# Optimization experiments

Measured on AMD Instinct MI355X. Metric: run time of the kernel, lower is better.

The kernel has to match this reference:

```python
import jax, jax.numpy as jnp
import numpy as np
from jax import lax


def binarize(x):
    # sign() binarization with straight-through estimator (identity backward),
    # matching the BNN .data in-place trick in BinarizeConv2d / bilinear.
    return x + lax.stop_gradient(jnp.sign(x) - x)


def maxpool2x2(x):
    # NCHW 2x2 max pool, stride 2
    return lax.reduce_window(x, -jnp.inf, lax.max,
                             (1, 1, 2, 2), (1, 1, 2, 2), 'VALID')


def conv2d(x, w):
    # NCHW / OIHW valid conv, stride 1
    return lax.conv_general_dilated(x, w, (1, 1), 'VALID',
                                    dimension_numbers=('NCHW', 'OIHW', 'NCHW'))


def setup_inputs() -> dict:
    key = jax.random.key(0)
    ks = jax.random.split(key, 6)
    B = 16384
    x = jax.random.normal(ks[0], (B, 1, 32, 32), dtype=jnp.float32)
    w1 = jax.random.normal(ks[1], (6, 1, 5, 5), dtype=jnp.float32) * 0.2
    w2 = jax.random.normal(ks[2], (16, 6, 5, 5), dtype=jnp.float32) * 0.08
    wfc1 = jax.random.normal(ks[3], (120, 400), dtype=jnp.float32) * 0.05
    wfc2 = jax.random.normal(ks[4], (84, 120), dtype=jnp.float32) * 0.09
    wfc3 = jax.random.normal(ks[5], (10, 84), dtype=jnp.float32) * 0.1
    return {'x': x, 'w1': w1, 'w2': w2, 'wfc1': wfc1, 'wfc2': wfc2, 'wfc3': wfc3}


def reference(x, w1, w2, wfc1, wfc2, wfc3):
    # conv1 (binarized input + weights) -> pool
    h = maxpool2x2(conv2d(binarize(x), binarize(w1)))          # [B,6,14,14]
    # conv2 -> pool
    h = maxpool2x2(conv2d(binarize(h), binarize(w2)))          # [B,16,5,5]
    h = h.reshape(h.shape[0], -1)                              # [B,400]
    h = binarize(h) @ binarize(wfc1).T                         # [B,120]
    h = binarize(h) @ binarize(wfc2).T                         # [B,84]
    h = binarize(h) @ binarize(wfc3).T                         # [B,10]
    return h
```

## Files before the change

### kernel.cpp

```cpp
#include <hip/hip_runtime.h>
#include <hip/hip_bf16.h>

typedef unsigned int u32;
typedef unsigned short u16;
typedef unsigned long long u64;

#define OC1 0
#define OC2 8
#define WCONV 104
#define OF1 104
#define OF2 2024
#define OF3 2664
#define WTOT 2704

__global__ void pack_w(const float* __restrict__ w1, const float* __restrict__ w2,
                       const float* __restrict__ f1, const float* __restrict__ f2,
                       const float* __restrict__ f3, u64* __restrict__ P) {
    int g = blockIdx.x * 256 + threadIdx.x;
    if (g < 1920) {
        int j = g / 15, w = g % 15;
        u64 v = 0;
        if (w < 14 && j < 120) {
            bool sp = (w >= 7); int k = sp ? w - 7 : w;
            for (int f = 0; f < 4; f++) {
                int p = 4 * k + f;
                if (p < 25)
                    for (int ch = 0; ch < 16; ch++) {
                        float x = f1[j * 400 + ch * 25 + p];
                        bool b = sp ? (x < 0.0f) : (x != 0.0f);
                        if (b) v |= 1ull << (f * 16 + ch);
                    }
            }
        }
        P[OF1 + g] = v;
    } else if (g < 2560) {
        int g2 = g - 1920, j = g2 / 5, w = g2 % 5;
        u64 v = 0;
        if (w < 4 && j < 84) {
            bool sp = (w >= 2); int h = w & 1;
            for (int b = 0; b < 64; b++) {
                int k = h * 64 + b;
                if (k < 120) {
                    float x = f2[j * 120 + k];
                    bool bb = sp ? (x < 0.0f) : (x != 0.0f);
                    if (bb) v |= 1ull << b;
                }
            }
        }
        P[OF2 + g2] = v;
    } else if (g < 2600) {
        int g3 = g - 2560, j = g3 / 4, w = g3 % 4;
        bool sp = (w >= 2); int h = w & 1;
        u64 v = 0;
        for (int b = 0; b < 64; b++) {
            int k = h * 64 + b;
            if (k < 84) {
                float x = f3[j * 84 + k];
                bool bb = sp ? (x < 0.0f) : (x != 0.0f);
                if (bb) v |= 1ull << b;
            }
        }
        P[OF3 + g3] = v;
    } else if (g < 2696) {
        int c = g - 2600, ch = c / 6, w = c % 6;
        bool sp = (w >= 3); int wp = w % 3;
        u64 v = 0;
        for (int half = 0; half < 2; half++) {
            int r = 2 * wp + half;
            if (r < 5) {
                u32 rowv = 0;
                for (int ci = 0; ci < 6; ci++)
                    for (int cc = 0; cc < 5; cc++) {
                        float x = w2[((ch * 6 + ci) * 5 + r) * 5 + cc];
                        bool b = sp ? (x < 0.0f) : (x != 0.0f);
                        int bit = (ci < 3) ? (5 * ci + cc) : (15 + 5 * (ci - 3) + cc);
                        if (b) rowv |= 1u << bit;
                    }
                v |= (u64)rowv << (32 * half);
            }
        }
        P[OC2 + ch * 6 + (sp ? 3 : 0) + wp] = v;
    } else if (g < 2702) {
        int c = g - 2696;
        int pair = c % 3; bool sp = (c >= 3);
        u64 v = 0;
        for (int half = 0; half < 2; half++) {
            int ch = 2 * pair + half;
            u32 wd = 0;
            for (int r = 0; r < 5; r++)
                for (int cc = 0; cc < 5; cc++) {
                    float x = w1[ch * 25 + r * 5 + cc];
                    bool b = sp ? (x < 0.0f) : (x != 0.0f);
                    if (b) wd |= 1u << (6 * r + cc);
                }
            v |= (u64)wd << (32 * half);
        }
        P[OC1 + (sp ? 3 : 0) + pair] = v;
    }
}

#define G 8

__device__ __forceinline__ u32 sgnb(int v) { return (u32)v >> 31; }
__device__ __forceinline__ u32 nzb(int v)  { return (u32)(v | -v) >> 31; }
#define WB() __builtin_amdgcn_wave_barrier()

__global__ __launch_bounds__(256, 8) void lenet_main(const float* __restrict__ X,
                                                     const u64* __restrict__ P,
                                                     float* __restrict__ out) {
    __shared__ u32 xs[G][32], xn[G][32];
    __shared__ u64 h1An[G][14], h1As[G][14], h1Bn[G][14], h1Bs[G][14];
    __shared__ u64 h2n[G][7], h2s[G][7];
    __shared__ u64 f1s[G][2], f1n[G][2], f2s[G][2], f2n[G][2];

    const int tid = threadIdx.x;
    const int wid = tid >> 6, lane = tid & 63;
    const int img0 = blockIdx.x * G;
    const int liA = wid * 2, liB = liA + 1;
    const int li0 = liA;

    const float4* X4 = (const float4*)(X + (size_t)img0 * 1024);

    float4 rvA[4];
    #pragma unroll
    for (int it = 0; it < 4; it++) rvA[it] = X4[liA * 256 + it * 64 + lane];

    u64 db;
    {
        bool bad = false;
        if (lane < 51) {
            u64 w, exp;
            if (lane < 48) {
                int ch = lane / 3, k = lane % 3;
                w = P[OC2 + ch * 6 + k];
                exp = (k < 2) ? 0x3FFFFFFF3FFFFFFFull : 0x000000003FFFFFFFull;
            } else {
                w = P[OC1 + (lane - 48)];
                exp = 0x1F7DF7DF1F7DF7DFull;
            }
            bad = (w != exp);
        }
        db = __ballot(bad);
    }

    auto conv1_fast = [&](int li) {
        const int px = lane & 15;
        const int pxe = px < 14 ? px : 13;
        const int tt = 2 * pxe;
        const int g = lane >> 4;
        u64 c1s0 = P[OC1 + 3], c1s1 = P[OC1 + 4], c1s2 = P[OC1 + 5];
        #pragma unroll
        for (int it = 0; it < 4; it++) {
            int seg = it * 4 + g;
            int py = seg < 14 ? seg : 13;
            int oy = 2 * py;
            u32 rs[6];
            #pragma unroll
            for (int k = 0; k < 6; k++) rs[k] = xs[li][oy + k];
            u32 W6a = 0;
            #pragma unroll
            for (int r = 0; r < 5; r++) W6a |= ((rs[r] >> tt) & 63u) << (6 * r);
            u32 W6b = (W6a >> 6) | (((rs[5] >> tt) & 63u) << 24);
            u32 cnt[6];
            #pragma unroll
            for (int c = 0; c < 6; c++) cnt[c] = 255;
            #pragma unroll
            for (int dy = 0; dy < 2; dy++) {
                u32 base = dy ? W6b : W6a;
                #pragma unroll
                for (int dx = 0; dx < 2; dx++) {
                    u32 w = (dx ? (base >> 1) : base) & 0x1F7DF7DFu;
                    u64 W = ((u64)w << 32) | w;
                    u64 t0 = W ^ c1s0;
                    cnt[0] = min(cnt[0], (u32)__popc((u32)t0));
                    cnt[1] = min(cnt[1], (u32)__popc((u32)(t0 >> 32)));
                    u64 t1 = W ^ c1s1;
                    cnt[2] = min(cnt[2], (u32)__popc((u32)t1));
                    cnt[3] = min(cnt[3], (u32)__popc((u32)(t1 >> 32)));
                    u64 t2w = W ^ c1s2;
                    cnt[4] = min(cnt[4], (u32)__popc((u32)t2w));
                    cnt[5] = min(cnt[5], (u32)__popc((u32)(t2w >> 32)));
                }
            }
            u64 bS[6];
            #pragma unroll
            for (int c = 0; c < 6; c++) bS[c] = __ballot(cnt[c] >= 13);
            if (px == 0 && seg < 14) {
                int sh = lane & 48;
                u64 rAs = ((bS[0] >> sh) & 0x3FFF) | (((bS[1] >> sh) & 0x3FFF) << 16) | (((bS[2] >> sh) & 0x3FFF) << 32);
                u64 rBs = ((bS[3] >> sh) & 0x3FFF) | (((bS[4] >> sh) & 0x3FFF) << 16) | (((bS[5] >> sh) & 0x3FFF) << 32);
                h1As[li][seg] = rAs; h1Bs[li][seg] = rBs;
            }
        }
    };
    auto conv1_slow = [&](int li) {
        const int px = lane & 15;
        const int pxe = px < 14 ? px : 13;
        const int tt = 2 * pxe;
        const int g = lane >> 4;
        for (int it = 0; it < 4; it++) {
            int seg = it * 4 + g;
            int py = seg < 14 ? seg : 13;
            int oy = 2 * py;
            int best[6];
            for (int c = 0; c < 6; c++) best[c] = -1000;
            for (int dy = 0; dy < 2; dy++)
                for (int dx = 0; dx < 2; dx++) {
                    u32 wn = 0, ws = 0;
                    for (int r = 0; r < 5; r++) {
                        u32 an = xn[li][oy + dy + r], as = xs[li][oy + dy + r];
                        wn |= ((an >> (tt + dx)) & 31u) << (6 * r);
                        ws |= ((as >> (tt + dx)) & 31u) << (6 * r);
                    }
                    u64 Wn = ((u64)wn << 32) | wn;
                    u64 Ws = ((u64)ws << 32) | ws;
                    for (int p = 0; p < 3; p++) {
                        u64 cn = P[OC1 + p], cs = P[OC1 + 3 + p];
                        u64 m  = Wn & cn;
                        u64 mx = m & (Ws ^ cs);
                        int a0 = __popc((u32)m) - 2 * __popc((u32)mx);
                        int a1 = __popc((u32)(m >> 32)) - 2 * __popc((u32)(mx >> 32));
                        best[2 * p]     = max(best[2 * p], a0);
                        best[2 * p + 1] = max(best[2 * p + 1], a1);
                    }
                }
            u64 bS[6], bN[6];
            for (int c = 0; c < 6; c++) {
                bS[c] = __ballot(best[c] < 0);
                bN[c] = __ballot(best[c] != 0);
            }
            if (px == 0 && seg < 14) {
                int sh = lane & 48;
                u64 rAs = ((bS[0] >> sh) & 0x3FFF) | (((bS[1] >> sh) & 0x3FFF) << 16) | (((bS[2] >> sh) & 0x3FFF) << 32);
                u64 rAn = ((bN[0] >> sh) & 0x3FFF) | (((bN[1] >> sh) & 0x3FFF) << 16) | (((bN[2] >> sh) & 0x3FFF) << 32);
                u64 rBs = ((bS[3] >> sh) & 0x3FFF) | (((bS[4] >> sh) & 0x3FFF) << 16) | (((bS[5] >> sh) & 0x3FFF) << 32);
                u64 rBn = ((bN[3] >> sh) & 0x3FFF) | (((bN[4] >> sh) & 0x3FFF) << 16) | (((bN[5] >> sh) & 0x3FFF) << 32);
                h1As[li][seg] = rAs; h1An[li][seg] = rAn;
                h1Bs[li][seg] = rBs; h1Bn[li][seg] = rBn;
            }
        }
    };

    u32 naccA = 15u;
    #pragma unroll
    for (int it = 0; it < 4; it++) {
        float4 v = rvA[it];
        u32 s = (v.x < 0.0f ? 1u : 0u) | (v.y < 0.0f ? 2u : 0u)
              | (v.z < 0.0f ? 4u : 0u) | (v.w < 0.0f ? 8u : 0u);
        u32 n = (v.x != 0.0f ? 1u : 0u) | (v.y != 0.0f ? 2u : 0u)
              | (v.z != 0.0f ? 4u : 0u) | (v.w != 0.0f ? 8u : 0u);
        naccA &= n;
        u32 sw = s << (4 * (lane & 7));
        sw |= __shfl_xor((int)sw, 1); sw |= __shfl_xor((int)sw, 2); sw |= __shfl_xor((int)sw, 4);
        if ((lane & 7) == 0) xs[liA][it * 8 + (lane >> 3)] = sw;
    }
    const bool fpA = ((__ballot(naccA != 15u) | db) == 0);
    if (!fpA) {
        #pragma unroll
        for (int it = 0; it < 4; it++) {
            float4 v = rvA[it];
            u32 n = (v.x != 0.0f ? 1u : 0u) | (v.y != 0.0f ? 2u : 0u)
                  | (v.z != 0.0f ? 4u : 0u) | (v.w != 0.0f ? 8u : 0u);
            u32 nw = n << (4 * (lane & 7));
            nw |= __shfl_xor((int)nw, 1); nw |= __shfl_xor((int)nw, 2); nw |= __shfl_xor((int)nw, 4);
            if ((lane & 7) == 0) xn[liA][it * 8 + (lane >> 3)] = nw;
        }
    }

    float4 rvB[4];
    #pragma unroll
    for (int it = 0; it < 4; it++) rvB[it] = X4[liB * 256 + it * 64 + lane];

    WB();
    if (fpA) conv1_fast(liA); else conv1_slow(liA);

    u32 naccB = 15u;
    #pragma unroll
    for (int it = 0; it < 4; it++) {
        float4 v = rvB[it];
        u32 s = (v.x < 0.0f ? 1u : 0u) | (v.y < 0.0f ? 2u : 0u)
              | (v.z < 0.0f ? 4u : 0u) | (v.w < 0.0f ? 8u : 0u);
        u32 n = (v.x != 0.0f ? 1u : 0u) | (v.y != 0.0f ? 2u : 0u)
              | (v.z != 0.0f ? 4u : 0u) | (v.w != 0.0f ? 8u : 0u);
        naccB &= n;
        u32 sw = s << (4 * (lane & 7));
        sw |= __shfl_xor((int)sw, 1); sw |= __shfl_xor((int)sw, 2); sw |= __shfl_xor((int)sw, 4);
        if ((lane & 7) == 0) xs[liB][it * 8 + (lane >> 3)] = sw;
    }
    const bool fpB = ((__ballot(naccB != 15u) | db) == 0);
    if (!fpB) {
        #pragma unroll
        for (int it = 0; it < 4; it++) {
            float4 v = rvB[it];
            u32 n = (v.x != 0.0f ? 1u : 0u) | (v.y != 0.0f ? 2u : 0u)
                  | (v.z != 0.0f ? 4u : 0u) | (v.w != 0.0f ? 8u : 0u);
            u32 nw = n << (4 * (lane & 7));
            nw |= __shfl_xor((int)nw, 1); nw |= __shfl_xor((int)nw, 2); nw |= __shfl_xor((int)nw, 4);
            if ((lane & 7) == 0) xn[liB][it * 8 + (lane >> 3)] = nw;
        }
    }
    WB();
    if (fpB) conv1_fast(liB); else conv1_slow(liB);
    WB();

    if (lane < 6) {
        int li = li0 + (lane >= 3 ? 1 : 0); int t = lane % 3;
        ((u16*)h2n[li])[25 + t] = 0; ((u16*)h2s[li])[25 + t] = 0;
    }
    if (lane < 50) {
        int im = lane >= 25 ? 1 : 0, p = lane - 25 * im, li = li0 + im;
        bool cfast = im ? fpB : fpA;
        int py = p / 5, px2 = p % 5;
        int y0 = 2 * py;
        if (cfast) {
            u32 dsg[2][6];
            for (int r = 0; r < 6; r++) {
                u64 a = h1As[li][y0 + r], b = h1Bs[li][y0 + r];
                for (int dx = 0; dx < 2; dx++) {
                    int t2 = 2 * px2 + dx;
                    u64 as = a >> t2, bs = b >> t2;
                    dsg[dx][r] = (((u32)as & 31u) | ((u32)(as >> 11) & 0x3E0u) | ((u32)(as >> 22) & 0x7C00u))
                               | ((((u32)bs & 31u) | ((u32)(bs >> 11) & 0x3E0u) | ((u32)(bs >> 22) & 0x7C00u)) << 15);
                }
            }
            u64 Ps[2][4];
            for (int dx = 0; dx < 2; dx++)
                for (int r = 0; r < 4; r++)
                    Ps[dx][r] = (u64)dsg[dx][r] | ((u64)dsg[dx][r + 1] << 32);
            u32 sb = 0, nb = 0;
            #pragma unroll 4
            for (int ch = 0; ch < 16; ch++) {
                u64 w0s = P[OC2 + ch * 6 + 3], w1s = P[OC2 + ch * 6 + 4];
                u32 w2s = (u32)P[OC2 + ch * 6 + 5];
                u32 mn = 255;
                for (int dy = 0; dy < 2; dy++)
                    for (int dx = 0; dx < 2; dx++) {
                        u64 t0 = Ps[dx][dy] ^ w0s, t1 = Ps[dx][dy + 2] ^ w1s;
                        u32 t2v = (dy ? dsg[dx][5] : dsg[dx][4]) ^ w2s;
                        u32 c = __popcll(t0) + __popcll(t1) + __popc(t2v);
                        mn = min(mn, c);
                    }
                sb |= (mn >= 76 ? 1u : 0u) << ch;
                nb |= (mn != 75 ? 1u : 0u) << ch;
            }
            ((u16*)h2s[li])[p] = (u16)sb;
            ((u16*)h2n[li])[p] = (u16)nb;
        } else {
            u32 dn[2][6], dsg[2][6];
            for (int r = 0; r < 6; r++) {
                u64 a_n = h1An[li][y0 + r], a_s = h1As[li][y0 + r];
                u64 b_n = h1Bn[li][y0 + r], b_s = h1Bs[li][y0 + r];
                for (int dx = 0; dx < 2; dx++) {
                    int t2 = 2 * px2 + dx;
                    u64 an = a_n >> t2, as = a_s >> t2, bn = b_n >> t2, bs = b_s >> t2;
                    dn[dx][r]  = (((u32)an & 31u) | ((u32)(an >> 11) & 0x3E0u) | ((u32)(an >> 22) & 0x7C00u))
                               | ((((u32)bn & 31u) | ((u32)(bn >> 11) & 0x3E0u) | ((u32)(bn >> 22) & 0x7C00u)) << 15);
                    dsg[dx][r] = (((u32)as & 31u) | ((u32)(as >> 11) & 0x3E0u) | ((u32)(as >> 22) & 0x7C00u))
                               | ((((u32)bs & 31u) | ((u32)(bs >> 11) & 0x3E0u) | ((u32)(bs >> 22) & 0x7C00u)) << 15);
                }
            }
            u64 Pn[2][4], Ps[2][4];
            for (int dx = 0; dx < 2; dx++)
                for (int r = 0; r < 4; r++) {
                    Pn[dx][r] = (u64)dn[dx][r]  | ((u64)dn[dx][r + 1]  << 32);
                    Ps[dx][r] = (u64)dsg[dx][r] | ((u64)dsg[dx][r + 1] << 32);
                }
            u32 sb = 0, nb = 0;
            #pragma unroll 4
            for (int ch = 0; ch < 16; ch++) {
                u64 w0n = P[OC2 + ch * 6 + 0], w1n = P[OC2 + ch * 6 + 1];
                u32 w2n = (u32)P[OC2 + ch * 6 + 2];
                u64 w0s = P[OC2 + ch * 6 + 3], w1s = P[OC2 + ch * 6 + 4];
                u32 w2s = (u32)P[OC2 + ch * 6 + 5];
                int am = -1000000;
                for (int dy = 0; dy < 2; dy++)
                    for (int dx = 0; dx < 2; dx++) {
                        u64 m0 = Pn[dx][dy] & w0n, m1 = Pn[dx][dy + 2] & w1n;
                        u32 m2 = (dy ? dn[dx][5] : dn[dx][4]) & w2n;
                        u64 x0 = m0 & (Ps[dx][dy] ^ w0s), x1 = m1 & (Ps[dx][dy + 2] ^ w1s);
                        u32 x2 = m2 & ((dy ? dsg[dx][5] : dsg[dx][4]) ^ w2s);
                        int v = __popcll(m0) + __popcll(m1) + __popc(m2)
                              - 2 * (__popcll(x0) + __popcll(x1) + __popc(x2));
                        am = max(am, v);
                    }
                sb |= sgnb(am) << ch;
                nb |= nzb(am) << ch;
            }
            ((u16*)h2s[li])[p] = (u16)sb;
            ((u16*)h2n[li])[p] = (u16)nb;
        }
    }
    WB();

    #pragma unroll
    for (int word = 0; word < 2; word++) {
        int j = word * 64 + lane;
        const u64* wj = P + OF1 + j * 15;
        u64 wn[7], ws[7];
        #pragma unroll
        for (int k = 0; k < 7; k++) { wn[k] = wj[k]; ws[k] = wj[7 + k]; }
        #pragma unroll
        for (int im = 0; im < 2; im++) {
            int li = li0 + im;
            int acc = 0;
            #pragma unroll
            for (int k = 0; k < 7; k++) {
                u64 m  = h2n[li][k] & wn[k];
                u64 mx = m & (h2s[li][k] ^ ws[k]);
                acc += __popcll(m) - 2 * __popcll(mx);
            }
            u64 bs = __ballot(acc < 0);
            u64 bn = __ballot(acc != 0);
            if (lane == 0) { f1s[li][word] = bs; f1n[li][word] = bn; }
        }
    }
    WB();

    #pragma unroll
    for (int word = 0; word < 2; word++) {
        int j = word * 64 + lane;
        const u64* wj = P + OF2 + j * 5;
        u64 a0 = wj[0], a1 = wj[1], s0 = wj[2], s1 = wj[3];
        #pragma unroll
        for (int im = 0; im < 2; im++) {
            int li = li0 + im;
            u64 m0 = f1n[li][0] & a0, m1 = f1n[li][1] & a1;
            u64 x0 = m0 & (f1s[li][0] ^ s0), x1 = m1 & (f1s[li][1] ^ s1);
            int acc = __popcll(m0) + __popcll(m1) - 2 * (__popcll(x0) + __popcll(x1));
            u64 bs = __ballot(acc < 0);
            u64 bn = __ballot(acc != 0);
            if (lane == 0) { f2s[li][word] = bs; f2n[li][word] = bn; }
        }
    }
    WB();

    if (lane < 32) {
        int im = lane >> 4, j = lane & 15, li = li0 + im;
        if (j < 10) {
            const u64* wj = P + OF3 + j * 4;
            u64 m0 = f2n[li][0] & wj[0], m1 = f2n[li][1] & wj[1];
            u64 x0 = m0 & (f2s[li][0] ^ wj[2]), x1 = m1 & (f2s[li][1] ^ wj[3]);
            int acc = __popcll(m0) + __popcll(m1) - 2 * (__popcll(x0) + __popcll(x1));
            out[(size_t)(img0 + li) * 10 + j] = (float)acc;
        }
    }
}

extern "C" void kernel_launch(void* const* d_in, const int* in_sizes, int n_in,
                              void* d_out, int out_size, void* d_ws, size_t ws_size,
                              hipStream_t stream) {
    const float* x    = (const float*)d_in[0];
    const float* w1   = (const float*)d_in[1];
    const float* w2   = (const float*)d_in[2];
    const float* wfc1 = (const float*)d_in[3];
    const float* wfc2 = (const float*)d_in[4];
    const float* wfc3 = (const float*)d_in[5];
    float* out = (float*)d_out;
    u64* P = (u64*)d_ws;

    int B = in_sizes[0] / 1024;

    pack_w<<<11, 256, 0, stream>>>(w1, w2, wfc1, wfc2, wfc3, P);
    lenet_main<<<B / G, 256, 0, stream>>>(x, P, out);
}
```

Measured before the change: 168.7 us.

## Prefetch second image directly into LDS via global_load_lds while computing first

Loads of the second image per wave now go straight into a new 16 KB shared staging buffer through global_load_lds issued at kernel start. They overlap with the first image's binarize and conv1, replacing the register-held float4 prefetch. The conv1 lambdas become macros and the nonzero mask is now always computed inline instead of in a conditional second pass. The added LDS use and a launch-bounds drop from 8 to 6 waves-per-EU trade occupancy for lower register pressure and memory-latency hiding.

New measurement: 149.1 us. -11.6%, faster.

```diff
diff --git a/kernel.cpp b/kernel.cpp
--- a/kernel.cpp
+++ b/kernel.cpp
@@ -105,9 +105,107 @@
 __device__ __forceinline__ u32 nzb(int v)  { return (u32)(v | -v) >> 31; }
 #define WB() __builtin_amdgcn_wave_barrier()
 
-__global__ __launch_bounds__(256, 8) void lenet_main(const float* __restrict__ X,
+#define GLOAD16(gp, lp) __builtin_amdgcn_global_load_lds( \
+    (const __attribute__((address_space(1))) void*)(gp), \
+    (__attribute__((address_space(3))) void*)(lp), 16, 0, 0)
+
+#define CONV1_FAST(LI) do {                                                   \
+    const int px_ = lane & 15;                                                \
+    const int pxe_ = px_ < 14 ? px_ : 13;                                     \
+    const int tt_ = 2 * pxe_;                                                 \
+    const int g_ = lane >> 4;                                                 \
+    u64 c1s0_ = P[OC1 + 3], c1s1_ = P[OC1 + 4], c1s2_ = P[OC1 + 5];           \
+    _Pragma("unroll")                                                         \
+    for (int it_ = 0; it_ < 4; it_++) {                                       \
+        int seg_ = it_ * 4 + g_;                                              \
+        int py_ = seg_ < 14 ? seg_ : 13;                                      \
+        int oy_ = 2 * py_;                                                    \
+        u32 rs0_ = xs[LI][oy_], rs1_ = xs[LI][oy_ + 1], rs2_ = xs[LI][oy_ + 2]; \
+        u32 rs3_ = xs[LI][oy_ + 3], rs4_ = xs[LI][oy_ + 4], rs5_ = xs[LI][oy_ + 5]; \
+        u32 W6a_ = ((rs0_ >> tt_) & 63u) | (((rs1_ >> tt_) & 63u) << 6)       \
+                 | (((rs2_ >> tt_) & 63u) << 12) | (((rs3_ >> tt_) & 63u) << 18) \
+                 | (((rs4_ >> tt_) & 63u) << 24);                             \
+        u32 W6b_ = (W6a_ >> 6) | (((rs5_ >> tt_) & 63u) << 24);               \
+        u32 c0_ = 255, c1_ = 255, c2_ = 255, c3_ = 255, c4_ = 255, c5_ = 255; \
+        _Pragma("unroll")                                                     \
+        for (int dy_ = 0; dy_ < 2; dy_++) {                                   \
+            u32 base_ = dy_ ? W6b_ : W6a_;                                    \
+            _Pragma("unroll")                                                 \
+            for (int dx_ = 0; dx_ < 2; dx_++) {                               \
+                u32 w_ = (dx_ ? (base_ >> 1) : base_) & 0x1F7DF7DFu;          \
+                u64 W_ = ((u64)w_ << 32) | w_;                                \
+                u64 t0_ = W_ ^ c1s0_;                                         \
+                c0_ = min(c0_, (u32)__popc((u32)t0_));                        \
+                c1_ = min(c1_, (u32)__popc((u32)(t0_ >> 32)));                \
+                u64 t1_ = W_ ^ c1s1_;                                         \
+                c2_ = min(c2_, (u32)__popc((u32)t1_));                        \
+                c3_ = min(c3_, (u32)__popc((u32)(t1_ >> 32)));                \
+                u64 t2_ = W_ ^ c1s2_;                                         \
+                c4_ = min(c4_, (u32)__popc((u32)t2_));                        \
+                c5_ = min(c5_, (u32)__popc((u32)(t2_ >> 32)));                \
+            }                                                                 \
+        }                                                                     \
+        u64 b0_ = __ballot(c0_ >= 13), b1_ = __ballot(c1_ >= 13);             \
+        u64 b2_ = __ballot(c2_ >= 13), b3_ = __ballot(c3_ >= 13);             \
+        u64 b4_ = __ballot(c4_ >= 13), b5_ = __ballot(c5_ >= 13);             \
+        if (px_ == 0 && seg_ < 14) {                                          \
+            int sh_ = lane & 48;                                              \
+            h1As[LI][seg_] = ((b0_ >> sh_) & 0x3FFF) | (((b1_ >> sh_) & 0x3FFF) << 16) | (((b2_ >> sh_) & 0x3FFF) << 32); \
+            h1Bs[LI][seg_] = ((b3_ >> sh_) & 0x3FFF) | (((b4_ >> sh_) & 0x3FFF) << 16) | (((b5_ >> sh_) & 0x3FFF) << 32); \
+        }                                                                     \
+    }                                                                         \
+} while (0)
+
+#define CONV1_SLOW(LI) do {                                                   \
+    const int px_ = lane & 15;                                                \
+    const int pxe_ = px_ < 14 ? px_ : 13;                                     \
+    const int tt_ = 2 * pxe_;                                                 \
+    const int g_ = lane >> 4;                                                 \
+    for (int it_ = 0; it_ < 4; it_++) {                                       \
+        int seg_ = it_ * 4 + g_;                                              \
+        int py_ = seg_ < 14 ? seg_ : 13;                                      \
+        int oy_ = 2 * py_;                                                    \
+        int best_[6];                                                         \
+        for (int c_ = 0; c_ < 6; c_++) best_[c_] = -1000;                     \
+        for (int dy_ = 0; dy_ < 2; dy_++)                                     \
+            for (int dx_ = 0; dx_ < 2; dx_++) {                               \
+                u32 wn_ = 0, ws_ = 0;                                         \
+                for (int r_ = 0; r_ < 5; r_++) {                              \
+                    u32 an_ = xn[LI][oy_ + dy_ + r_], as_ = xs[LI][oy_ + dy_ + r_]; \
+                    wn_ |= ((an_ >> (tt_ + dx_)) & 31u) << (6 * r_);          \
+                    ws_ |= ((as_ >> (tt_ + dx_)) & 31u) << (6 * r_);          \
+                }                                                             \
+                u64 Wn_ = ((u64)wn_ << 32) | wn_;                             \
+                u64 Ws_ = ((u64)ws_ << 32) | ws_;                             \
+                for (int p_ = 0; p_ < 3; p_++) {                              \
+                    u64 cn_ = P[OC1 + p_], cs_ = P[OC1 + 3 + p_];             \
+                    u64 m_ = Wn_ & cn_;                                       \
+                    u64 mx_ = m_ & (Ws_ ^ cs_);                               \
+                    int a0_ = __popc((u32)m_) - 2 * __popc((u32)mx_);         \
+                    int a1_ = __popc((u32)(m_ >> 32)) - 2 * __popc((u32)(mx_ >> 32)); \
+                    best_[2 * p_]     = max(best_[2 * p_], a0_);              \
+                    best_[2 * p_ + 1] = max(best_[2 * p_ + 1], a1_);          \
+                }                                                             \
+            }                                                                 \
+        u64 bS_[6], bN_[6];                                                   \
+        for (int c_ = 0; c_ < 6; c_++) {                                      \
+            bS_[c_] = __ballot(best_[c_] < 0);                                \
+            bN_[c_] = __ballot(best_[c_] != 0);                               \
+        }                                                                     \
+        if (px_ == 0 && seg_ < 14) {                                          \
+            int sh_ = lane & 48;                                              \
+            h1As[LI][seg_] = ((bS_[0] >> sh_) & 0x3FFF) | (((bS_[1] >> sh_) & 0x3FFF) << 16) | (((bS_[2] >> sh_) & 0x3FFF) << 32); \
+            h1An[LI][seg_] = ((bN_[0] >> sh_) & 0x3FFF) | (((bN_[1] >> sh_) & 0x3FFF) << 16) | (((bN_[2] >> sh_) & 0x3FFF) << 32); \
+            h1Bs[LI][seg_] = ((bS_[3] >> sh_) & 0x3FFF) | (((bS_[4] >> sh_) & 0x3FFF) << 16) | (((bS_[5] >> sh_) & 0x3FFF) << 32); \
+            h1Bn[LI][seg_] = ((bN_[3] >> sh_) & 0x3FFF) | (((bN_[4] >> sh_) & 0x3FFF) << 16) | (((bN_[5] >> sh_) & 0x3FFF) << 32); \
+        }                                                                     \
+    }                                                                         \
+} while (0)
+
+__global__ __launch_bounds__(256, 6) void lenet_main(const float* __restrict__ X,
                                                      const u64* __restrict__ P,
                                                      float* __restrict__ out) {
+    __shared__ __align__(16) float stage[4][1024];
     __shared__ u32 xs[G][32], xn[G][32];
     __shared__ u64 h1An[G][14], h1As[G][14], h1Bn[G][14], h1Bs[G][14];
     __shared__ u64 h2n[G][7], h2s[G][7];
@@ -121,9 +219,13 @@
 
     const float4* X4 = (const float4*)(X + (size_t)img0 * 1024);
 
-    float4 rvA[4];
-    #pragma unroll
-    for (int it = 0; it < 4; it++) rvA[it] = X4[liA * 256 + it * 64 + lane];
+    {
+        const float* gB = X + ((size_t)img0 + liB) * 1024;
+        GLOAD16(gB + 0 * 256 + lane * 4, &stage[wid][0 * 256]);
+        GLOAD16(gB + 1 * 256 + lane * 4, &stage[wid][1 * 256]);
+        GLOAD16(gB + 2 * 256 + lane * 4, &stage[wid][2 * 256]);
+        GLOAD16(gB + 3 * 256 + lane * 4, &stage[wid][3 * 256]);
+    }
 
     u64 db;
     {
@@ -143,164 +245,44 @@
         db = __ballot(bad);
     }
 
-    auto conv1_fast = [&](int li) {
-        const int px = lane & 15;
-        const int pxe = px < 14 ? px : 13;
-        const int tt = 2 * pxe;
-        const int g = lane >> 4;
-        u64 c1s0 = P[OC1 + 3], c1s1 = P[OC1 + 4], c1s2 = P[OC1 + 5];
-        #pragma unroll
-        for (int it = 0; it < 4; it++) {
-            int seg = it * 4 + g;
-            int py = seg < 14 ? seg : 13;
-            int oy = 2 * py;
-            u32 rs[6];
-            #pragma unroll
-            for (int k = 0; k < 6; k++) rs[k] = xs[li][oy + k];
-            u32 W6a = 0;
-            #pragma unroll
-            for (int r = 0; r < 5; r++) W6a |= ((rs[r] >> tt) & 63u) << (6 * r);
-            u32 W6b = (W6a >> 6) | (((rs[5] >> tt) & 63u) << 24);
-            u32 cnt[6];
-            #pragma unroll
-            for (int c = 0; c < 6; c++) cnt[c] = 255;
-            #pragma unroll
-            for (int dy = 0; dy < 2; dy++) {
-                u32 base = dy ? W6b : W6a;
-                #pragma unroll
-                for (int dx = 0; dx < 2; dx++) {
-                    u32 w = (dx ? (base >> 1) : base) & 0x1F7DF7DFu;
-                    u64 W = ((u64)w << 32) | w;
-                    u64 t0 = W ^ c1s0;
-                    cnt[0] = min(cnt[0], (u32)__popc((u32)t0));
-                    cnt[1] = min(cnt[1], (u32)__popc((u32)(t0 >> 32)));
-                    u64 t1 = W ^ c1s1;
-                    cnt[2] = min(cnt[2], (u32)__popc((u32)t1));
-                    cnt[3] = min(cnt[3], (u32)__popc((u32)(t1 >> 32)));
-                    u64 t2w = W ^ c1s2;
-                    cnt[4] = min(cnt[4], (u32)__popc((u32)t2w));
-                    cnt[5] = min(cnt[5], (u32)__popc((u32)(t2w >> 32)));
-                }
-            }
-            u64 bS[6];
-            #pragma unroll
-            for (int c = 0; c < 6; c++) bS[c] = __ballot(cnt[c] >= 13);
-            if (px == 0 && seg < 14) {
-                int sh = lane & 48;
-                u64 rAs = ((bS[0] >> sh) & 0x3FFF) | (((bS[1] >> sh) & 0x3FFF) << 16) | (((bS[2] >> sh) & 0x3FFF) << 32);
-                u64 rBs = ((bS[3] >> sh) & 0x3FFF) | (((bS[4] >> sh) & 0x3FFF) << 16) | (((bS[5] >> sh) & 0x3FFF) << 32);
-                h1As[li][seg] = rAs; h1Bs[li][seg] = rBs;
-            }
-        }
-    };
-    auto conv1_slow = [&](int li) {
-        const int px = lane & 15;
-        const int pxe = px < 14 ? px : 13;
-        const int tt = 2 * pxe;
-        const int g = lane >> 4;
-        for (int it = 0; it < 4; it++) {
-            int seg = it * 4 + g;
-            int py = seg < 14 ? seg : 13;
-            int oy = 2 * py;
-            int best[6];
-            for (int c = 0; c < 6; c++) best[c] = -1000;
-            for (int dy = 0; dy < 2; dy++)
-                for (int dx = 0; dx < 2; dx++) {
-                    u32 wn = 0, ws = 0;
-                    for (int r = 0; r < 5; r++) {
-                        u32 an = xn[li][oy + dy + r], as = xs[li][oy + dy + r];
-                        wn |= ((an >> (tt + dx)) & 31u) << (6 * r);
-                        ws |= ((as >> (tt + dx)) & 31u) << (6 * r);
-                    }
-                    u64 Wn = ((u64)wn << 32) | wn;
-                    u64 Ws = ((u64)ws << 32) | ws;
-                    for (int p = 0; p < 3; p++) {
-                        u64 cn = P[OC1 + p], cs = P[OC1 + 3 + p];
-                        u64 m  = Wn & cn;
-                        u64 mx = m & (Ws ^ cs);
-                        int a0 = __popc((u32)m) - 2 * __popc((u32)mx);
-                        int a1 = __popc((u32)(m >> 32)) - 2 * __popc((u32)(mx >> 32));
-                        best[2 * p]     = max(best[2 * p], a0);
-                        best[2 * p + 1] = max(best[2 * p + 1], a1);
-                    }
-                }
-            u64 bS[6], bN[6];
-            for (int c = 0; c < 6; c++) {
-                bS[c] = __ballot(best[c] < 0);
-                bN[c] = __ballot(best[c] != 0);
-            }
-            if (px == 0 && seg < 14) {
-                int sh = lane & 48;
-                u64 rAs = ((bS[0] >> sh) & 0x3FFF) | (((bS[1] >> sh) & 0x3FFF) << 16) | (((bS[2] >> sh) & 0x3FFF) << 32);
-                u64 rAn = ((bN[0] >> sh) & 0x3FFF) | (((bN[1] >> sh) & 0x3FFF) << 16) | (((bN[2] >> sh) & 0x3FFF) << 32);
-                u64 rBs = ((bS[3] >> sh) & 0x3FFF) | (((bS[4] >> sh) & 0x3FFF) << 16) | (((bS[5] >> sh) & 0x3FFF) << 32);
-                u64 rBn = ((bN[3] >> sh) & 0x3FFF) | (((bN[4] >> sh) & 0x3FFF) << 16) | (((bN[5] >> sh) & 0x3FFF) << 32);
-                h1As[li][seg] = rAs; h1An[li][seg] = rAn;
-                h1Bs[li][seg] = rBs; h1Bn[li][seg] = rBn;
-            }
-        }
-    };
-
     u32 naccA = 15u;
     #pragma unroll
     for (int it = 0; it < 4; it++) {
-        float4 v = rvA[it];
+        float4 v = X4[liA * 256 + it * 64 + lane];
         u32 s = (v.x < 0.0f ? 1u : 0u) | (v.y < 0.0f ? 2u : 0u)
               | (v.z < 0.0f ? 4u : 0u) | (v.w < 0.0f ? 8u : 0u);
         u32 n = (v.x != 0.0f ? 1u : 0u) | (v.y != 0.0f ? 2u : 0u)
               | (v.z != 0.0f ? 4u : 0u) | (v.w != 0.0f ? 8u : 0u);
         naccA &= n;
-        u32 sw = s << (4 * (lane & 7));
+        u32 sw = s << (4 * (lane & 7)), nw = n << (4 * (lane & 7));
         sw |= __shfl_xor((int)sw, 1); sw |= __shfl_xor((int)sw, 2); sw |= __shfl_xor((int)sw, 4);
-        if ((lane & 7) == 0) xs[liA][it * 8 + (lane >> 3)] = sw;
+        nw |= __shfl_xor((int)nw, 1); nw |= __shfl_xor((int)nw, 2); nw |= __shfl_xor((int)nw, 4);
+        if ((lane & 7) == 0) { xs[liA][it * 8 + (lane >> 3)] = sw; xn[liA][it * 8 + (lane >> 3)] = nw; }
     }
     const bool fpA = ((__ballot(naccA != 15u) | db) == 0);
-    if (!fpA) {
-        #pragma unroll
-        for (int it = 0; it < 4; it++) {
-            float4 v = rvA[it];
-            u32 n = (v.x != 0.0f ? 1u : 0u) | (v.y != 0.0f ? 2u : 0u)
-                  | (v.z != 0.0f ? 4u : 0u) | (v.w != 0.0f ? 8u : 0u);
-            u32 nw = n << (4 * (lane & 7));
-            nw |= __shfl_xor((int)nw, 1); nw |= __shfl_xor((int)nw, 2); nw |= __shfl_xor((int)nw, 4);
-            if ((lane & 7) == 0) xn[liA][it * 8 + (lane >> 3)] = nw;
-        }
-    }
-
-    float4 rvB[4];
-    #pragma unroll
-    for (int it = 0; it < 4; it++) rvB[it] = X4[liB * 256 + it * 64 + lane];
-
-    WB();
-    if (fpA) conv1_fast(liA); else conv1_slow(liA);
-
+    WB();
+
+    if (fpA) CONV1_FAST(liA); else CONV1_SLOW(liA);
+
+    asm volatile("s_waitcnt vmcnt(0)" ::: "memory");
+    __builtin_amdgcn_sched_barrier(0);
     u32 naccB = 15u;
     #pragma unroll
     for (int it = 0; it < 4; it++) {
-        float4 v = rvB[it];
+        float4 v = *(const float4*)&stage[wid][it * 256 + lane * 4];
         u32 s = (v.x < 0.0f ? 1u : 0u) | (v.y < 0.0f ? 2u : 0u)
               | (v.z < 0.0f ? 4u : 0u) | (v.w < 0.0f ? 8u : 0u);
         u32 n = (v.x != 0.0f ? 1u : 0u) | (v.y != 0.0f ? 2u : 0u)
               | (v.z != 0.0f ? 4u : 0u) | (v.w != 0.0f ? 8u : 0u);
         naccB &= n;
-        u32 sw = s << (4 * (lane & 7));
+        u32 sw = s << (4 * (lane & 7)), nw = n << (4 * (lane & 7));
         sw |= __shfl_xor((int)sw, 1); sw |= __shfl_xor((int)sw, 2); sw |= __shfl_xor((int)sw, 4);
-        if ((lane & 7) == 0) xs[liB][it * 8 + (lane >> 3)] = sw;
+        nw |= __shfl_xor((int)nw, 1); nw |= __shfl_xor((int)nw, 2); nw |= __shfl_xor((int)nw, 4);
+        if ((lane & 7) == 0) { xs[liB][it * 8 + (lane >> 3)] = sw; xn[liB][it * 8 + (lane >> 3)] = nw; }
     }
     const bool fpB = ((__ballot(naccB != 15u) | db) == 0);
-    if (!fpB) {
-        #pragma unroll
-        for (int it = 0; it < 4; it++) {
-            float4 v = rvB[it];
-            u32 n = (v.x != 0.0f ? 1u : 0u) | (v.y != 0.0f ? 2u : 0u)
-                  | (v.z != 0.0f ? 4u : 0u) | (v.w != 0.0f ? 8u : 0u);
-            u32 nw = n << (4 * (lane & 7));
-            nw |= __shfl_xor((int)nw, 1); nw |= __shfl_xor((int)nw, 2); nw |= __shfl_xor((int)nw, 4);
-            if ((lane & 7) == 0) xn[liB][it * 8 + (lane >> 3)] = nw;
-        }
-    }
-    WB();
-    if (fpB) conv1_fast(liB); else conv1_slow(liB);
+    WB();
+    if (fpB) CONV1_FAST(liB); else CONV1_SLOW(liB);
     WB();
 
     if (lane < 6) {
```
